# Kernel tuning notes

Measured on AMD Instinct MI355X. Metric: run time of the kernel, lower is better.

The kernel has to match this reference:

```python
import math
import jax, jax.numpy as jnp
import numpy as np

B, L, DM = 2, 1024, 1024
STATE, EXPAND, CONV, DTR = 16, 2, 4, 8
INNER = DM * EXPAND          # 2048
NFFT = L // 2 + 1            # 513


def _silu(v):
    return v * jax.nn.sigmoid(v)


def setup_inputs() -> dict:
    key = jax.random.key(0)
    ks = jax.random.split(key, 12)
    s = lambda k, shape, sc=0.02: (jax.random.normal(k, shape, jnp.float32) * sc)
    # dt_proj bias initialized like the torch module: exp(U(0,1)*(log dt_max - log dt_min) + log dt_min)
    inv_dt = jnp.exp(jax.random.uniform(ks[10], (INNER,), jnp.float32)
                     * (math.log(0.1) - math.log(0.001)) + math.log(0.001))
    return {
        "x": jax.random.normal(ks[0], (B, L, DM), jnp.float32),
        "in_proj_w": s(ks[1], (2 * INNER, DM)),
        "conv_w": s(ks[2], (INNER, 1, CONV), 0.1),      # depthwise conv kernel
        "conv_b": jnp.zeros((INNER,), jnp.float32),
        "A_log": jnp.tile(jnp.log(jnp.arange(1, STATE + 1, dtype=jnp.float32)), (INNER, 1)),
        "D": jnp.ones((INNER,), jnp.float32),
        "x_proj_w": s(ks[3], (DTR + 2 * STATE, INNER)),
        "dt_proj_w": s(ks[4], (INNER, DTR)),
        "dt_proj_b": inv_dt,
        "filter_real": s(ks[5], (INNER, NFFT)),
        "filter_imag": s(ks[6], (INNER, NFFT)),
        "spectral_decay": jnp.ones((INNER,), jnp.float32) * 0.01,
        "fusion_w": s(ks[7], (INNER, 2 * INNER)),
        "fusion_b": jnp.zeros((INNER,), jnp.float32),
        "out_proj_w": s(ks[8], (DM, INNER)),
        "ln_gamma": jnp.ones((DM,), jnp.float32),
        "ln_beta": jnp.zeros((DM,), jnp.float32),
    }


def reference(x, in_proj_w, conv_w, conv_b, A_log, D, x_proj_w, dt_proj_w, dt_proj_b,
              filter_real, filter_imag, spectral_decay, fusion_w, fusion_b,
              out_proj_w, ln_gamma, ln_beta):
    residual = x
    xz = x @ in_proj_w.T                                   # [B,L,2*INNER]
    x_inner, z = xz[..., :INNER], xz[..., INNER:]
    z = _silu(z)

    # ---- SSM path ----
    xc = jnp.swapaxes(x_inner, 1, 2)                       # [B,E,L]
    xc = jax.lax.conv_general_dilated(
        xc, conv_w, (1,), [(CONV - 1, 0)],                 # causal depthwise conv (pad-left == torch pad + truncate)
        dimension_numbers=("NCH", "OIH", "NCH"),
        feature_group_count=INNER) + conv_b[None, :, None]
    x_conv = jnp.swapaxes(_silu(xc), 1, 2)                 # [B,L,E]

    x_dbc = x_conv @ x_proj_w.T                            # [B,L,DTR+2S]
    dt_x = x_dbc[..., :DTR]
    Bm = x_dbc[..., DTR:DTR + STATE]                       # [B,L,S]
    Cm = x_dbc[..., DTR + STATE:]                          # [B,L,S]
    dt = jax.nn.softplus(dt_x @ dt_proj_w.T + dt_proj_b)   # [B,L,E]
    A = -jnp.exp(A_log)                                    # [E,S]
    dA = jnp.exp(dt[..., None] * A)                        # [B,L,E,S]
    dBx = (dt * x_conv)[..., None] * Bm[:, :, None, :]     # [B,L,E,S]

    def step(h, inp):
        dA_t, dBx_t, C_t = inp
        h = dA_t * h + dBx_t                               # [B,E,S]
        return h, jnp.einsum('bes,bs->be', h, C_t)

    h0 = jnp.zeros((B, INNER, STATE), x.dtype)
    _, ys = jax.lax.scan(step, h0,
                         (jnp.swapaxes(dA, 0, 1), jnp.swapaxes(dBx, 0, 1), jnp.swapaxes(Cm, 0, 1)))
    y_ssm = jnp.swapaxes(ys, 0, 1) + x_conv * D            # [B,L,E]

    # ---- Spectral path ----
    xf = jnp.fft.rfft(jnp.swapaxes(x_inner, 1, 2), axis=-1)        # [B,E,NFFT]
    freqs = jnp.linspace(0.0, 1.0, NFFT)
    filt = (filter_real + 1j * filter_imag) * jnp.exp(-spectral_decay[:, None] * freqs[None, :])
    y_spec = jnp.swapaxes(jnp.fft.irfft(xf * filt[None], n=L, axis=-1), 1, 2)  # [B,L,E]

    # ---- Gated fusion ----
    g = jax.nn.sigmoid(jnp.concatenate([y_ssm, y_spec], -1) @ fusion_w.T + fusion_b)
    y = g * y_ssm + (1.0 - g) * y_spec
    y = y * z
    out = y @ out_proj_w.T + residual                      # [B,L,DM]

    mu = out.mean(-1, keepdims=True)
    var = out.var(-1, keepdims=True)
    return (out - mu) / jnp.sqrt(var + 1e-5) * ln_gamma + ln_beta
```

## Files before the change

### kernel.cpp

```cpp
#include <hip/hip_runtime.h>
#include <math.h>

#define B_ 2
#define L_ 1024
#define DM_ 1024
#define STATE_ 16
#define CONV_ 4
#define DTR_ 8
#define INNER_ 2048
#define M_ (B_*L_)
#define MD_ (B_*INNER_)
#define NFFT_ 513
#define NFP_ 1152
#define NCH_ 32
#define CHL_ 32
#define SK_ 32
#define KSL_ (2048/SK_)

typedef unsigned short u16;
typedef __attribute__((ext_vector_type(8))) short short8;
typedef __attribute__((ext_vector_type(8))) __bf16 bf16x8;
typedef __attribute__((ext_vector_type(4))) float f32x4;

__device__ __forceinline__ float frcp_(float x) { return __builtin_amdgcn_rcpf(x); }
__device__ __forceinline__ float fexp_(float x) { return __expf(x); }
__device__ __forceinline__ float fsigm_(float x) { return frcp_(1.f + __expf(-x)); }
__device__ __forceinline__ float fsilu_(float x) { return x * frcp_(1.f + __expf(-x)); }
__device__ __forceinline__ float fsoftplus_(float v) {
  return (v > 20.f) ? v : __logf(1.f + __expf(v));
}
__device__ __forceinline__ u16 f2bf(float f) {
  union { float f; unsigned u; } v; v.f = f;
  unsigned r = v.u + 0x7fffu + ((v.u >> 16) & 1u);
  return (u16)(r >> 16);
}
__device__ __forceinline__ float bf2f(u16 h) {
  union { unsigned u; float f; } v; v.u = ((unsigned)h) << 16;
  return v.f;
}
__device__ __forceinline__ void gload16(const void* g, void* l) {
  __builtin_amdgcn_global_load_lds(
      (const __attribute__((address_space(1))) unsigned*)g,
      (__attribute__((address_space(3))) unsigned*)l, 16, 0, 0);
}
__device__ __forceinline__ f32x4 mfma_bf16(short8 a, short8 b, f32x4 c) {
  return __builtin_amdgcn_mfma_f32_16x16x32_bf16(
      __builtin_bit_cast(bf16x8, a), __builtin_bit_cast(bf16x8, b), c, 0, 0, 0);
}

#define CVT_N0 2097152
#define CVT_N1 6291456
#define CVT_N2 14680064
#define CVT_NT 16777216
__global__ __launch_bounds__(256) void cvt4_k(
    const float* __restrict__ s0, const float* __restrict__ s1,
    const float* __restrict__ s2, const float* __restrict__ s3,
    u16* __restrict__ out)
{
  int i = (blockIdx.x*256 + threadIdx.x) * 4;
  const float* src; int off;
  if (i < CVT_N0)      { src = s0; off = 0; }
  else if (i < CVT_N1) { src = s1; off = CVT_N0; }
  else if (i < CVT_N2) { src = s2; off = CVT_N1; }
  else                 { src = s3; off = CVT_N2; }
  float4 v = *(const float4*)(src + (i - off));
  ushort4 o;
  o.x = f2bf(v.x); o.y = f2bf(v.y); o.z = f2bf(v.z); o.w = f2bf(v.w);
  *(ushort4*)(out + i) = o;
}

template<int TM, int TN, int EPI, int YCH>
__global__ __launch_bounds__((TM/64)*(TN/32)*64) void mgemm_k(
    const u16* __restrict__ Ab, const u16* __restrict__ Bb,
    void* __restrict__ Cout, int K, int ldc,
    const float* __restrict__ aux0, u16* __restrict__ aux1,
    const float* __restrict__ aux2, const float* __restrict__ aux3,
    int gx, int gy)
{
  constexpr int WN   = TN/32;
  constexpr int NW   = (TM/64)*WN;
  constexpr int NTHR = NW*64;
  __shared__ __align__(16) u16 As[2][TM*64];
  __shared__ __align__(16) u16 Bs[2][TN*64];
  const int t = threadIdx.x;
  const int lane = t & 63;
  const int w = t >> 6;
  const int wm = w / WN, wn = w % WN;

  const int nwg = gx * gy;
  const int bid = blockIdx.x;
  const int lid = (bid & 7) * (nwg >> 3) + (bid >> 3);
  int bx, by;
  if (YCH) { by = lid / gx; bx = lid - by*gx; }
  else     { bx = lid / gy; by = lid - bx*gy; }
  const int M0 = by * TM, N0 = bx * TN;

  f32x4 acc[4][2] = {};

  auto stage = [&](int buf, int k0) {
    #pragma unroll
    for (int q = 0; q < TM*8/NTHR; q++) {
      int u = q*NTHR + t;
      int row = u >> 3, gpr = u & 7;
      int grp = gpr ^ (row & 7);
      gload16(Ab + (size_t)(M0+row)*K + k0 + grp*8, &As[buf][u*8]);
    }
    #pragma unroll
    for (int q = 0; q < TN*8/NTHR; q++) {
      int u = q*NTHR + t;
      int row = u >> 3, gpr = u & 7;
      int grp = gpr ^ (row & 7);
      gload16(Bb + (size_t)(N0+row)*K + k0 + grp*8, &Bs[buf][u*8]);
    }
  };

  stage(0, 0);
  const int nk = K >> 6;
  for (int ks = 0; ks < nk; ks++) {
    const int buf = ks & 1;
    __syncthreads();
    if (ks + 1 < nk) stage(buf ^ 1, (ks + 1) << 6);
    const u16* Asb = As[buf];
    const u16* Bsb = Bs[buf];
    #pragma unroll
    for (int kk = 0; kk < 2; kk++) {
      const int quad = lane >> 4;
      const int grp = kk*4 + quad;
      short8 af[4], bfr[2];
      #pragma unroll
      for (int i = 0; i < 4; i++) {
        int row = wm*64 + i*16 + (lane & 15);
        af[i] = *(const short8*)&Asb[(row*8 + (grp ^ (row & 7)))*8];
      }
      #pragma unroll
      for (int j = 0; j < 2; j++) {
        int row = wn*32 + j*16 + (lane & 15);
        bfr[j] = *(const short8*)&Bsb[(row*8 + (grp ^ (row & 7)))*8];
      }
      #pragma unroll
      for (int i = 0; i < 4; i++)
        #pragma unroll
        for (int j = 0; j < 2; j++)
          acc[i][j] = mfma_bf16(af[i], bfr[j], acc[i][j]);
    }
  }

  #pragma unroll
  for (int i = 0; i < 4; i++) {
    int mbase = M0 + wm*64 + i*16 + (lane >> 4)*4;
    #pragma unroll
    for (int j = 0; j < 2; j++) {
      int n = N0 + wn*32 + j*16 + (lane & 15);
      #pragma unroll
      for (int r = 0; r < 4; r++) {
        int m = mbase + r;
        float v = acc[i][j][r];
        if (EPI == 0) {
          ((float*)Cout)[(size_t)m*ldc + n] = v;
        } else if (EPI == 1) {
          float g  = fsigm_(v + aux0[n]);
          float ys = bf2f(aux1[(size_t)m*4096 + n]);
          float yp = bf2f(aux1[(size_t)m*4096 + 2048 + n]);
          float z  = aux2[(size_t)m*4096 + 2048 + n];
          ((u16*)Cout)[(size_t)m*ldc + n] = f2bf((g*ys + (1.f-g)*yp)*fsilu_(z));
        } else if (EPI == 2) {
          ((float*)Cout)[(size_t)m*ldc + n] = v + aux2[(size_t)m*ldc + n];
        } else if (EPI == 3) {
          float pv = __shfl_xor(v, 1, 64);
          int f = n >> 1;
          float outv = 0.f;
          if (f < NFFT_) {
            int c = m & (INNER_-1);
            float d  = fexp_(-aux2[c] * (float)f * (1.f/512.f));
            float wr = aux0[c*NFFT_+f]*d, wi = aux3[c*NFFT_+f]*d;
            float a = (n & 1) ? pv : v;
            float b = (n & 1) ? v : pv;
            outv = (n & 1) ? (a*wi + b*wr) : (a*wr - b*wi);
          }
          ((u16*)Cout)[(size_t)m*ldc + n] = f2bf(outv);
        } else if (EPI == 5) {
          ((float*)Cout)[(size_t)m*ldc + n] = v;
          if (n < 2048) {
            int b2 = m >> 10, l2 = m & 1023;
            aux1[((size_t)(b2*2048 + n) << 10) + l2] = f2bf(v);
          }
        } else {
          int b2 = m >> 11, c2 = m & (INNER_-1);
          ((u16*)Cout)[((size_t)((b2 << 10) + n) << 12) + 2048 + c2] = f2bf(v);
        }
      }
    }
  }
}

__global__ __launch_bounds__(256) void xproj_k(
    const float* __restrict__ xconv, const float* __restrict__ W,
    float* __restrict__ part)
{
  __shared__ float Bs[40][KSL_+4];
  const int sk = blockIdx.x, mt = blockIdx.y;
  const int k0 = sk*KSL_;
  for (int i = threadIdx.x; i < 40*KSL_; i += 256) {
    int n = i >> 6, k = i & (KSL_-1);
    Bs[n][k] = W[(size_t)n*2048 + k0 + k];
  }
  __syncthreads();
  const int m = mt*256 + threadIdx.x;
  const float* arow = xconv + (size_t)m*2048 + k0;
  float acc[40];
  #pragma unroll
  for (int j=0;j<40;j++) acc[j]=0.f;
  for (int k = 0; k < KSL_; k += 4) {
    float4 a = *(const float4*)(arow + k);
    #pragma unroll
    for (int j = 0; j < 40; j++) {
      float4 b = *(const float4*)&Bs[j][k];
      acc[j] += a.x*b.x + a.y*b.y + a.z*b.z + a.w*b.w;
    }
  }
  float* o = part + ((size_t)sk*M_ + m)*40;
  #pragma unroll
  for (int j = 0; j < 10; j++)
    *(float4*)(o + j*4) = make_float4(acc[j*4], acc[j*4+1], acc[j*4+2], acc[j*4+3]);
}

__global__ __launch_bounds__(256) void xpred_k(const float* __restrict__ part,
                                               float* __restrict__ xdbc)
{
  int i = blockIdx.x*256 + threadIdx.x;
  float s = 0.f;
  #pragma unroll
  for (int sk = 0; sk < SK_; sk++) s += part[(size_t)sk*81920 + i];
  xdbc[i] = s;
}

__global__ __launch_bounds__(256) void conv_silu_k(
    const float* __restrict__ xz, const float* __restrict__ cw,
    const float* __restrict__ cb, float* __restrict__ xc)
{
  int idx = blockIdx.x*256 + threadIdx.x;
  int c = idx & (INNER_-1);
  int g = idx >> 11;
  int b = g >> 7;
  int lb = (g & 127) * 8;
  float w0=cw[c*4+0], w1=cw[c*4+1], w2=cw[c*4+2], w3=cw[c*4+3];
  float bias = cb[c];
  float v[11];
  #pragma unroll
  for (int j = 0; j < 11; j++) {
    int l = lb - 3 + j;
    v[j] = (l >= 0) ? xz[((size_t)((b << 10) + l))*4096 + c] : 0.f;
  }
  #pragma unroll
  for (int j = 0; j < 8; j++) {
    float s = bias + w0*v[j] + w1*v[j+1] + w2*v[j+2] + w3*v[j+3];
    xc[((size_t)((b << 10) + lb + j))*INNER_ + c] = fsilu_(s);
  }
}

__global__ __launch_bounds__(256) void scan1_k(
    const float* __restrict__ xdbc, const float* __restrict__ xconv,
    const float* __restrict__ A_log, const float* __restrict__ dtw,
    const float* __restrict__ dtb, float* __restrict__ Pq)
{
  int idx = blockIdx.x*256 + threadIdx.x;
  int e  = idx & (INNER_-1);
  int bc = idx >> 11;
  int ch = bc & (NCH_-1);
  int b  = bc >> 5;
  float A[STATE_];
  #pragma unroll
  for (int s=0;s<STATE_;s++) A[s] = -fexp_(A_log[e*STATE_+s]);
  float w[DTR_];
  #pragma unroll
  for (int r=0;r<DTR_;r++) w[r] = dtw[e*DTR_+r];
  float bias = dtb[e];
  float h[STATE_] = {};
  float sdt = 0.f;
  int mbase = b*L_ + ch*CHL_;
  float dtx[DTR_], Bv[STATE_], xcv;
  {
    const float* row = xdbc + (size_t)mbase*40;
    #pragma unroll
    for (int r=0;r<DTR_;r++) dtx[r] = row[r];
    #pragma unroll
    for (int s=0;s<STATE_;s++) Bv[s] = row[8+s];
    xcv = xconv[(size_t)mbase*INNER_ + e];
  }
  for (int l=0;l<CHL_;l++) {
    float ndtx[DTR_], nBv[STATE_], nxcv = 0.f;
    if (l+1 < CHL_) {
      const float* nrow = xdbc + (size_t)(mbase+l+1)*40;
      #pragma unroll
      for (int r=0;r<DTR_;r++) ndtx[r] = nrow[r];
      #pragma unroll
      for (int s=0;s<STATE_;s++) nBv[s] = nrow[8+s];
      nxcv = xconv[(size_t)(mbase+l+1)*INNER_ + e];
    } else {
      #pragma unroll
      for (int r=0;r<DTR_;r++) ndtx[r] = 0.f;
      #pragma unroll
      for (int s=0;s<STATE_;s++) nBv[s] = 0.f;
    }
    float v = bias;
    #pragma unroll
    for (int r=0;r<DTR_;r++) v += dtx[r]*w[r];
    float dt = fsoftplus_(v);
    sdt += dt;
    float dx = dt * xcv;
    #pragma unroll
    for (int s=0;s<STATE_;s++) {
      float dA = fexp_(dt*A[s]);
      h[s] = dA*h[s] + dx*Bv[s];
    }
    #pragma unroll
    for (int r=0;r<DTR_;r++) dtx[r] = ndtx[r];
    #pragma unroll
    for (int s=0;s<STATE_;s++) Bv[s] = nBv[s];
    xcv = nxcv;
  }
  float* o = Pq + (size_t)idx*32;
  #pragma unroll
  for (int s=0;s<STATE_;s++) { o[s] = fexp_(A[s]*sdt); o[16+s] = h[s]; }
}

__global__ __launch_bounds__(256) void scan2_k(float* __restrict__ Pq)
{
  int idx = blockIdx.x*256 + threadIdx.x;
  int s = idx & 15;
  int e = (idx >> 4) & (INNER_-1);
  int b = idx >> 15;
  float h = 0.f;
  for (int ch = 0; ch < NCH_; ch++) {
    size_t base = ((size_t)(b*NCH_+ch)*INNER_ + e)*32;
    float p = Pq[base + s];
    float q = Pq[base + 16 + s];
    Pq[base + 16 + s] = h;
    h = p*h + q;
  }
}

__global__ __launch_bounds__(256) void scan3_k(
    const float* __restrict__ xdbc, const float* __restrict__ xconv,
    const float* __restrict__ A_log, const float* __restrict__ dtw,
    const float* __restrict__ dtb, const float* __restrict__ Dp,
    const float* __restrict__ Pq, u16* __restrict__ ycat)
{
  int idx = blockIdx.x*256 + threadIdx.x;
  int e  = idx & (INNER_-1);
  int bc = idx >> 11;
  int ch = bc & (NCH_-1);
  int b  = bc >> 5;
  float A[STATE_];
  #pragma unroll
  for (int s=0;s<STATE_;s++) A[s] = -fexp_(A_log[e*STATE_+s]);
  float w[DTR_];
  #pragma unroll
  for (int r=0;r<DTR_;r++) w[r] = dtw[e*DTR_+r];
  float bias = dtb[e];
  float Dv = Dp[e];
  float h[STATE_];
  const float* hi = Pq + (size_t)idx*32 + 16;
  #pragma unroll
  for (int s=0;s<STATE_;s++) h[s] = hi[s];
  int mbase = b*L_ + ch*CHL_;
  float dtx[DTR_], Bv[STATE_], Cv[STATE_], xcv;
  {
    const float* row = xdbc + (size_t)mbase*40;
    #pragma unroll
    for (int r=0;r<DTR_;r++) dtx[r] = row[r];
    #pragma unroll
    for (int s=0;s<STATE_;s++) { Bv[s] = row[8+s]; Cv[s] = row[24+s]; }
    xcv = xconv[(size_t)mbase*INNER_ + e];
  }
  for (int l=0;l<CHL_;l++) {
    float ndtx[DTR_], nBv[STATE_], nCv[STATE_], nxcv = 0.f;
    if (l+1 < CHL_) {
      const float* nrow = xdbc + (size_t)(mbase+l+1)*40;
      #pragma unroll
      for (int r=0;r<DTR_;r++) ndtx[r] = nrow[r];
      #pragma unroll
      for (int s=0;s<STATE_;s++) { nBv[s] = nrow[8+s]; nCv[s] = nrow[24+s]; }
      nxcv = xconv[(size_t)(mbase+l+1)*INNER_ + e];
    } else {
      #pragma unroll
      for (int r=0;r<DTR_;r++) ndtx[r] = 0.f;
      #pragma unroll
      for (int s=0;s<STATE_;s++) { nBv[s] = 0.f; nCv[s] = 0.f; }
    }
    float v = bias;
    #pragma unroll
    for (int r=0;r<DTR_;r++) v += dtx[r]*w[r];
    float dt = fsoftplus_(v);
    float dx = dt * xcv;
    float y = 0.f;
    #pragma unroll
    for (int s=0;s<STATE_;s++) {
      float dA = fexp_(dt*A[s]);
      h[s] = dA*h[s] + dx*Bv[s];
      y += h[s]*Cv[s];
    }
    ycat[(size_t)(mbase+l)*4096 + e] = f2bf(y + xcv*Dv);
    #pragma unroll
    for (int r=0;r<DTR_;r++) dtx[r] = ndtx[r];
    #pragma unroll
    for (int s=0;s<STATE_;s++) { Bv[s] = nBv[s]; Cv[s] = nCv[s]; }
    xcv = nxcv;
  }
}

__global__ __launch_bounds__(256) void genWdftb_k(u16* __restrict__ W) {
  int idx = blockIdx.x*256 + threadIdx.x;
  int l = idx & (L_-1);
  int col = idx >> 10;
  float v = 0.f;
  int f = col >> 1;
  if (f < NFFT_) {
    int ph = (l*f) & (L_-1);
    float th = (float)ph * (6.283185307179586f / (float)L_);
    v = (col & 1) ? -__sinf(th) : __cosf(th);
  }
  W[idx] = f2bf(v);
}

__global__ __launch_bounds__(256) void genWinvb_k(u16* __restrict__ W) {
  int idx = blockIdx.x*256 + threadIdx.x;
  int r = idx % NFP_;
  int l = idx / NFP_;
  int f = r >> 1;
  float v = 0.f;
  if (f < NFFT_) {
    bool edge = (f == 0) || (f == 512);
    float sc = (edge ? 1.f : 2.f) / (float)L_;
    int ph = (f*l) & (L_-1);
    float th = (float)ph * (6.283185307179586f / (float)L_);
    if (r & 1) v = edge ? 0.f : -sc*__sinf(th);
    else       v = sc*__cosf(th);
  }
  W[idx] = f2bf(v);
}

__global__ __launch_bounds__(256) void ln_k(const float* __restrict__ inp,
    const float* __restrict__ gma, const float* __restrict__ bta,
    float* __restrict__ out)
{
  int m = blockIdx.x;
  const float* row = inp + (size_t)m*DM_;
  float s=0.f, s2=0.f;
  float v[4];
  #pragma unroll
  for (int j=0;j<4;j++) {
    v[j] = row[threadIdx.x + j*256];
    s += v[j]; s2 += v[j]*v[j];
  }
  #pragma unroll
  for (int off=32; off>=1; off>>=1) {
    s  += __shfl_down(s, off);
    s2 += __shfl_down(s2, off);
  }
  __shared__ float rs[4], rs2[4], stats[2];
  int wid = threadIdx.x >> 6;
  if ((threadIdx.x & 63) == 0) { rs[wid]=s; rs2[wid]=s2; }
  __syncthreads();
  if (threadIdx.x == 0) {
    float ts  = rs[0]+rs[1]+rs[2]+rs[3];
    float ts2 = rs2[0]+rs2[1]+rs2[2]+rs2[3];
    float mu  = ts/(float)DM_;
    float var = ts2/(float)DM_ - mu*mu;
    stats[0] = mu; stats[1] = rsqrtf(var + 1e-5f);
  }
  __syncthreads();
  float mu = stats[0], rstd = stats[1];
  #pragma unroll
  for (int j=0;j<4;j++) {
    int n = threadIdx.x + j*256;
    out[(size_t)m*DM_ + n] = (v[j]-mu)*rstd*gma[n] + bta[n];
  }
}

extern "C" void kernel_launch(void* const* d_in, const int* in_sizes, int n_in,
                              void* d_out, int out_size, void* d_ws, size_t ws_size,
                              hipStream_t stream)
{
  const float* x       = (const float*)d_in[0];
  const float* in_w    = (const float*)d_in[1];
  const float* conv_w  = (const float*)d_in[2];
  const float* conv_b  = (const float*)d_in[3];
  const float* A_log   = (const float*)d_in[4];
  const float* Dp      = (const float*)d_in[5];
  const float* xproj_w = (const float*)d_in[6];
  const float* dt_w    = (const float*)d_in[7];
  const float* dt_b    = (const float*)d_in[8];
  const float* f_re    = (const float*)d_in[9];
  const float* f_im    = (const float*)d_in[10];
  const float* s_dec   = (const float*)d_in[11];
  const float* fus_w   = (const float*)d_in[12];
  const float* fus_b   = (const float*)d_in[13];
  const float* out_w   = (const float*)d_in[14];
  const float* ln_g    = (const float*)d_in[15];
  const float* ln_b    = (const float*)d_in[16];
  float* out = (float*)d_out;

  float* ws    = (float*)d_ws;
  float* xz    = ws;
  float* xconv = xz    + 8388608;
  float* xdbc  = xconv + 4194304;
  float* Pq    = xdbc  + 81920;
  u16* ub      = (u16*)(Pq + 4194304);
  u16* xb      = ub;
  u16* inwb    = xb    + 2097152;
  u16* fuswb   = inwb  + 4194304;
  u16* outwb   = fuswb + 8388608;
  u16* xt      = outwb + 2097152;
  u16* Wb      = xt    + 4194304;
  u16* XFb     = Wb    + 1179648;
  u16* ycat    = XFb   + 4718592;
  u16* ycomb   = xt;
  float* outp  = xconv;
  float* part  = (float*)ycat;

  cvt4_k<<<CVT_NT/1024, 256, 0, stream>>>(x, in_w, fus_w, out_w, xb);

  mgemm_k<128,128,5,0><<<512, 512, 0, stream>>>(
      xb, inwb, xz, 1024, 4096, nullptr, xt, nullptr, nullptr, 32, 16);
  conv_silu_k<<<(M_*INNER_/8)/256, 256, 0, stream>>>(xz, conv_w, conv_b, xconv);
  xproj_k<<<dim3(SK_, M_/256), 256, 0, stream>>>(xconv, xproj_w, part);
  xpred_k<<<(M_*40)/256, 256, 0, stream>>>(part, xdbc);
  scan1_k<<<(B_*NCH_*INNER_)/256, 256, 0, stream>>>(xdbc, xconv, A_log, dt_w, dt_b, Pq);
  scan2_k<<<(B_*INNER_*STATE_)/256, 256, 0, stream>>>(Pq);
  scan3_k<<<(B_*NCH_*INNER_)/256, 256, 0, stream>>>(xdbc, xconv, A_log, dt_w, dt_b, Dp, Pq, ycat);
  genWdftb_k<<<(NFP_*1024)/256, 256, 0, stream>>>(Wb);
  mgemm_k<128,64,3,1><<<576, 256, 0, stream>>>(
      xt, Wb, XFb, 1024, NFP_, f_re, nullptr, s_dec, f_im, 18, 32);
  genWinvb_k<<<(NFP_*1024)/256, 256, 0, stream>>>(Wb);
  mgemm_k<128,64,6,1><<<512, 256, 0, stream>>>(
      XFb, Wb, ycat, NFP_, 0, nullptr, nullptr, nullptr, nullptr, 16, 32);
  mgemm_k<128,64,1,0><<<512, 256, 0, stream>>>(
      ycat, fuswb, ycomb, 4096, 2048, fus_b, ycat, xz, nullptr, 32, 16);
  mgemm_k<64,64,2,1><<<512, 128, 0, stream>>>(
      ycomb, outwb, outp, 2048, 1024, nullptr, nullptr, x, nullptr, 16, 32);
  ln_k<<<M_, 256, 0, stream>>>(outp, ln_g, ln_b, out);
}
```

Measured before the change: 412.8 us.

## Overlap side kernels with GEMMs via extra blocks and trim DFT padding

Folds the DFT-matrix generation, causal conv+SiLU, inverse-DFT matrix generation and x_proj split-K into extra thread blocks appended to the GEMM launches, so independent work runs concurrently with the matmuls and several launches disappear. It also shrinks the padded frequency dimension from 1152 to 1088 columns, removing wasted GEMM work, and halves the x_proj split-K count, which reduces partial-sum traffic. Buffers are re-aliased (Winv into xb, part into inwb), so correctness now depends on those regions being dead when reused. Block-index dispatch adds a branch to every GEMM block.

```diff
diff --git a/kernel.cpp b/kernel.cpp
--- a/kernel.cpp
+++ b/kernel.cpp
@@ -11,10 +11,10 @@
 #define M_ (B_*L_)
 #define MD_ (B_*INNER_)
 #define NFFT_ 513
-#define NFP_ 1152
+#define NFP_ 1088
 #define NCH_ 32
 #define CHL_ 32
-#define SK_ 32
+#define SK_ 16
 #define KSL_ (2048/SK_)
 
 typedef unsigned short u16;
@@ -69,13 +69,101 @@
   *(ushort4*)(out + i) = o;
 }
 
-template<int TM, int TN, int EPI, int YCH>
+__device__ __forceinline__ void conv_body(int idx, const float* __restrict__ xz,
+    const float* __restrict__ cw, const float* __restrict__ cb,
+    float* __restrict__ xc)
+{
+  int c = idx & (INNER_-1);
+  int g = idx >> 11;
+  int b = g >> 7;
+  int lb = (g & 127) * 8;
+  float w0=cw[c*4+0], w1=cw[c*4+1], w2=cw[c*4+2], w3=cw[c*4+3];
+  float bias = cb[c];
+  float v[11];
+  #pragma unroll
+  for (int j = 0; j < 11; j++) {
+    int l = lb - 3 + j;
+    v[j] = (l >= 0) ? xz[((size_t)((b << 10) + l))*4096 + c] : 0.f;
+  }
+  #pragma unroll
+  for (int j = 0; j < 8; j++) {
+    float s = bias + w0*v[j] + w1*v[j+1] + w2*v[j+2] + w3*v[j+3];
+    xc[((size_t)((b << 10) + lb + j))*INNER_ + c] = fsilu_(s);
+  }
+}
+
+__device__ __forceinline__ void genWdft_body(int idx, u16* __restrict__ W)
+{
+  int l = idx & (L_-1);
+  int col = idx >> 10;
+  float v = 0.f;
+  int f = col >> 1;
+  if (f < NFFT_) {
+    int ph = (l*f) & (L_-1);
+    float th = (float)ph * (6.283185307179586f / (float)L_);
+    v = (col & 1) ? -__sinf(th) : __cosf(th);
+  }
+  W[idx] = f2bf(v);
+}
+
+__device__ __forceinline__ void genWinv_body(int idx, u16* __restrict__ W)
+{
+  int r = idx % NFP_;
+  int l = idx / NFP_;
+  int f = r >> 1;
+  float v = 0.f;
+  if (f < NFFT_) {
+    bool edge = (f == 0) || (f == 512);
+    float sc = (edge ? 1.f : 2.f) / (float)L_;
+    int ph = (f*l) & (L_-1);
+    float th = (float)ph * (6.283185307179586f / (float)L_);
+    if (r & 1) v = edge ? 0.f : -sc*__sinf(th);
+    else       v = sc*__cosf(th);
+  }
+  W[idx] = f2bf(v);
+}
+
+__device__ __forceinline__ void xproj_body(int eb,
+    const float* __restrict__ xconv, const float* __restrict__ W,
+    float* __restrict__ part, void* lds)
+{
+  float (*Bs)[KSL_+4] = (float(*)[KSL_+4])lds;
+  const int sk = eb & (SK_-1), mt = eb / SK_;
+  const int k0 = sk*KSL_;
+  for (int i = threadIdx.x; i < 40*KSL_; i += 256) {
+    int n = i / KSL_, k = i & (KSL_-1);
+    Bs[n][k] = W[(size_t)n*2048 + k0 + k];
+  }
+  __syncthreads();
+  const int m = mt*256 + threadIdx.x;
+  const float* arow = xconv + (size_t)m*2048 + k0;
+  float acc[40];
+  #pragma unroll
+  for (int j=0;j<40;j++) acc[j]=0.f;
+  for (int k = 0; k < KSL_; k += 4) {
+    float4 a = *(const float4*)(arow + k);
+    #pragma unroll
+    for (int j = 0; j < 40; j++) {
+      float4 b = *(const float4*)&Bs[j][k];
+      acc[j] += a.x*b.x + a.y*b.y + a.z*b.z + a.w*b.w;
+    }
+  }
+  float* o = part + ((size_t)sk*M_ + m)*40;
+  #pragma unroll
+  for (int j = 0; j < 10; j++)
+    *(float4*)(o + j*4) = make_float4(acc[j*4], acc[j*4+1], acc[j*4+2], acc[j*4+3]);
+}
+
+template<int TM, int TN, int EPI, int YCH, int AUX>
 __global__ __launch_bounds__((TM/64)*(TN/32)*64) void mgemm_k(
     const u16* __restrict__ Ab, const u16* __restrict__ Bb,
     void* __restrict__ Cout, int K, int ldc,
     const float* __restrict__ aux0, u16* __restrict__ aux1,
     const float* __restrict__ aux2, const float* __restrict__ aux3,
-    int gx, int gy)
+    int gx, int gy,
+    const float* __restrict__ ga, const float* __restrict__ gb,
+    const float* __restrict__ gc, float* __restrict__ go,
+    u16* __restrict__ gw)
 {
   constexpr int WN   = TN/32;
   constexpr int NW   = (TM/64)*WN;
@@ -83,6 +171,22 @@
   __shared__ __align__(16) u16 As[2][TM*64];
   __shared__ __align__(16) u16 Bs[2][TN*64];
   const int t = threadIdx.x;
+
+  if constexpr (AUX != 0) {
+    int eb = (int)blockIdx.x - gx*gy;
+    if (eb >= 0) {
+      if constexpr (AUX == 1) {
+        genWdft_body(eb*NTHR + t, gw);
+      } else if constexpr (AUX == 2) {
+        if (eb < 2048) conv_body(eb*256 + t, ga, gb, gc, go);
+        else           genWinv_body((eb - 2048)*256 + t, gw);
+      } else {
+        xproj_body(eb, ga, gb, go, (void*)&As[0][0]);
+      }
+      return;
+    }
+  }
+
   const int lane = t & 63;
   const int w = t >> 6;
   const int wm = w / WN, wn = w % WN;
@@ -193,37 +297,6 @@
   }
 }
 
-__global__ __launch_bounds__(256) void xproj_k(
-    const float* __restrict__ xconv, const float* __restrict__ W,
-    float* __restrict__ part)
-{
-  __shared__ float Bs[40][KSL_+4];
-  const int sk = blockIdx.x, mt = blockIdx.y;
-  const int k0 = sk*KSL_;
-  for (int i = threadIdx.x; i < 40*KSL_; i += 256) {
-    int n = i >> 6, k = i & (KSL_-1);
-    Bs[n][k] = W[(size_t)n*2048 + k0 + k];
-  }
-  __syncthreads();
-  const int m = mt*256 + threadIdx.x;
-  const float* arow = xconv + (size_t)m*2048 + k0;
-  float acc[40];
-  #pragma unroll
-  for (int j=0;j<40;j++) acc[j]=0.f;
-  for (int k = 0; k < KSL_; k += 4) {
-    float4 a = *(const float4*)(arow + k);
-    #pragma unroll
-    for (int j = 0; j < 40; j++) {
-      float4 b = *(const float4*)&Bs[j][k];
-      acc[j] += a.x*b.x + a.y*b.y + a.z*b.z + a.w*b.w;
-    }
-  }
-  float* o = part + ((size_t)sk*M_ + m)*40;
-  #pragma unroll
-  for (int j = 0; j < 10; j++)
-    *(float4*)(o + j*4) = make_float4(acc[j*4], acc[j*4+1], acc[j*4+2], acc[j*4+3]);
-}
-
 __global__ __launch_bounds__(256) void xpred_k(const float* __restrict__ part,
                                                float* __restrict__ xdbc)
 {
@@ -232,30 +305,6 @@
   #pragma unroll
   for (int sk = 0; sk < SK_; sk++) s += part[(size_t)sk*81920 + i];
   xdbc[i] = s;
-}
-
-__global__ __launch_bounds__(256) void conv_silu_k(
-    const float* __restrict__ xz, const float* __restrict__ cw,
-    const float* __restrict__ cb, float* __restrict__ xc)
-{
-  int idx = blockIdx.x*256 + threadIdx.x;
-  int c = idx & (INNER_-1);
-  int g = idx >> 11;
-  int b = g >> 7;
-  int lb = (g & 127) * 8;
-  float w0=cw[c*4+0], w1=cw[c*4+1], w2=cw[c*4+2], w3=cw[c*4+3];
-  float bias = cb[c];
-  float v[11];
-  #pragma unroll
-  for (int j = 0; j < 11; j++) {
-    int l = lb - 3 + j;
-    v[j] = (l >= 0) ? xz[((size_t)((b << 10) + l))*4096 + c] : 0.f;
-  }
-  #pragma unroll
-  for (int j = 0; j < 8; j++) {
-    float s = bias + w0*v[j] + w1*v[j+1] + w2*v[j+2] + w3*v[j+3];
-    xc[((size_t)((b << 10) + lb + j))*INNER_ + c] = fsilu_(s);
-  }
 }
 
 __global__ __launch_bounds__(256) void scan1_k(
@@ -407,37 +456,6 @@
     for (int s=0;s<STATE_;s++) { Bv[s] = nBv[s]; Cv[s] = nCv[s]; }
     xcv = nxcv;
   }
-}
-
-__global__ __launch_bounds__(256) void genWdftb_k(u16* __restrict__ W) {
-  int idx = blockIdx.x*256 + threadIdx.x;
-  int l = idx & (L_-1);
-  int col = idx >> 10;
-  float v = 0.f;
-  int f = col >> 1;
-  if (f < NFFT_) {
-    int ph = (l*f) & (L_-1);
-    float th = (float)ph * (6.283185307179586f / (float)L_);
-    v = (col & 1) ? -__sinf(th) : __cosf(th);
-  }
-  W[idx] = f2bf(v);
-}
-
-__global__ __launch_bounds__(256) void genWinvb_k(u16* __restrict__ W) {
-  int idx = blockIdx.x*256 + threadIdx.x;
-  int r = idx % NFP_;
-  int l = idx / NFP_;
-  int f = r >> 1;
-  float v = 0.f;
-  if (f < NFFT_) {
-    bool edge = (f == 0) || (f == 512);
-    float sc = (edge ? 1.f : 2.f) / (float)L_;
-    int ph = (f*l) & (L_-1);
-    float th = (float)ph * (6.283185307179586f / (float)L_);
-    if (r & 1) v = edge ? 0.f : -sc*__sinf(th);
-    else       v = sc*__cosf(th);
-  }
-  W[idx] = f2bf(v);
 }
 
 __global__ __launch_bounds__(256) void ln_k(const float* __restrict__ inp,
@@ -513,31 +531,33 @@
   u16* outwb   = fuswb + 8388608;
   u16* xt      = outwb + 2097152;
   u16* Wb      = xt    + 4194304;
-  u16* XFb     = Wb    + 1179648;
-  u16* ycat    = XFb   + 4718592;
+  u16* XFb     = Wb    + 1114112;
+  u16* ycat    = XFb   + 4456448;
   u16* ycomb   = xt;
+  u16* Winv    = xb;
   float* outp  = xconv;
-  float* part  = (float*)ycat;
+  float* part  = (float*)inwb;
 
   cvt4_k<<<CVT_NT/1024, 256, 0, stream>>>(x, in_w, fus_w, out_w, xb);
 
-  mgemm_k<128,128,5,0><<<512, 512, 0, stream>>>(
-      xb, inwb, xz, 1024, 4096, nullptr, xt, nullptr, nullptr, 32, 16);
-  conv_silu_k<<<(M_*INNER_/8)/256, 256, 0, stream>>>(xz, conv_w, conv_b, xconv);
-  xproj_k<<<dim3(SK_, M_/256), 256, 0, stream>>>(xconv, xproj_w, part);
+  mgemm_k<128,128,5,0,1><<<512 + (NFP_*1024)/512, 512, 0, stream>>>(
+      xb, inwb, xz, 1024, 4096, nullptr, xt, nullptr, nullptr, 32, 16,
+      nullptr, nullptr, nullptr, nullptr, Wb);
+  mgemm_k<128,64,3,1,2><<<544 + 2048 + (1024*NFP_)/256, 256, 0, stream>>>(
+      xt, Wb, XFb, 1024, NFP_, f_re, nullptr, s_dec, f_im, 17, 32,
+      xz, conv_w, conv_b, xconv, Winv);
+  mgemm_k<128,64,6,1,3><<<512 + SK_*8, 256, 0, stream>>>(
+      XFb, Winv, ycat, NFP_, 0, nullptr, nullptr, nullptr, nullptr, 16, 32,
+      xconv, xproj_w, nullptr, part, nullptr);
   xpred_k<<<(M_*40)/256, 256, 0, stream>>>(part, xdbc);
   scan1_k<<<(B_*NCH_*INNER_)/256, 256, 0, stream>>>(xdbc, xconv, A_log, dt_w, dt_b, Pq);
   scan2_k<<<(B_*INNER_*STATE_)/256, 256, 0, stream>>>(Pq);
   scan3_k<<<(B_*NCH_*INNER_)/256, 256, 0, stream>>>(xdbc, xconv, A_log, dt_w, dt_b, Dp, Pq, ycat);
-  genWdftb_k<<<(NFP_*1024)/256, 256, 0, stream>>>(Wb);
-  mgemm_k<128,64,3,1><<<576, 256, 0, stream>>>(
-      xt, Wb, XFb, 1024, NFP_, f_re, nullptr, s_dec, f_im, 18, 32);
-  genWinvb_k<<<(NFP_*1024)/256, 256, 0, stream>>>(Wb);
-  mgemm_k<128,64,6,1><<<512, 256, 0, stream>>>(
-      XFb, Wb, ycat, NFP_, 0, nullptr, nullptr, nullptr, nullptr, 16, 32);
-  mgemm_k<128,64,1,0><<<512, 256, 0, stream>>>(
-      ycat, fuswb, ycomb, 4096, 2048, fus_b, ycat, xz, nullptr, 32, 16);
-  mgemm_k<64,64,2,1><<<512, 128, 0, stream>>>(
-      ycomb, outwb, outp, 2048, 1024, nullptr, nullptr, x, nullptr, 16, 32);
+  mgemm_k<128,64,1,0,0><<<512, 256, 0, stream>>>(
+      ycat, fuswb, ycomb, 4096, 2048, fus_b, ycat, xz, nullptr, 32, 16,
+      nullptr, nullptr, nullptr, nullptr, nullptr);
+  mgemm_k<64,64,2,1,0><<<512, 128, 0, stream>>>(
+      ycomb, outwb, outp, 2048, 1024, nullptr, nullptr, x, nullptr, 16, 32,
+      nullptr, nullptr, nullptr, nullptr, nullptr);
   ln_k<<<M_, 256, 0, stream>>>(outp, ln_g, ln_b, out);
 }
```

Result: faster. 403.6 us (-2.2%).
